# Kernel tuning notes

Measured on AMD Instinct MI355X. Metric: run time of the kernel, lower is better.

## Reference

```python
import jax, jax.numpy as jnp
import numpy as np

N = 32768      # total nodes
E = 262144     # total edges
B = 32         # graphs in batch
NP = N // B    # nodes per graph (equal-sized graphs)
K = 820        # ceil(0.8 * NP), PyG TopKPooling k
H, C = 8, 64   # heads, per-head channels
NEG_SLOPE = 0.2


def setup_inputs() -> dict:
    key = jax.random.key(0)
    ks = jax.random.split(key, 12)
    s = 0.05
    return {
        "x": jax.random.normal(ks[0], (N, 256), jnp.float32),
        "edge_attr": jax.random.normal(ks[1], (E, 32), jnp.float32),
        "Wl": jax.random.normal(ks[2], (256, H * C), jnp.float32) * s,
        "bl": jax.random.normal(ks[3], (H * C,), jnp.float32) * s,
        "Wr": jax.random.normal(ks[4], (256, H * C), jnp.float32) * s,
        "br": jax.random.normal(ks[5], (H * C,), jnp.float32) * s,
        "We": jax.random.normal(ks[6], (32, H * C), jnp.float32) * s,
        "att": jax.random.normal(ks[7], (H, C), jnp.float32) * s,
        "bias": jax.random.normal(ks[8], (H * C,), jnp.float32) * s,
        "pool_w": jax.random.normal(ks[9], (H * C,), jnp.float32),
        "edge_index": jax.random.randint(ks[10], (2, E), 0, N, jnp.int32),
    }


def reference(x, edge_attr, Wl, bl, Wr, br, We, att, bias, pool_w, edge_index):
    src, dst = edge_index[0], edge_index[1]
    # GATv2Conv (eval mode, dropout off)
    xl = (x @ Wl + bl).reshape(N, H, C)   # x_j side (lin_l)
    xr = (x @ Wr + br).reshape(N, H, C)   # x_i side (lin_r)
    e = (edge_attr @ We).reshape(E, H, C)  # lin_edge, bias=False
    m = jax.nn.leaky_relu(xl[src] + xr[dst] + e, NEG_SLOPE)   # [E,H,C]
    alpha = jnp.einsum('ehc,hc->eh', m, att)                  # [E,H]
    amax = jax.ops.segment_max(alpha, dst, num_segments=N)
    ex = jnp.exp(alpha - amax[dst])
    denom = jax.ops.segment_sum(ex, dst, num_segments=N)
    alpha = ex / denom[dst]                                   # segment softmax over dst
    out = jax.ops.segment_sum(alpha[..., None] * xl[src], dst, num_segments=N)
    h = jax.nn.relu(out.reshape(N, H * C) + bias)             # [N,512]
    # TopKPooling: score = tanh(x.w / ||w||), keep top-k per graph, scale kept rows
    score = jnp.tanh(h @ pool_w / jnp.sqrt(jnp.sum(pool_w * pool_w)))
    vals, idx = jax.lax.top_k(score.reshape(B, NP), K)        # [B,K]
    hg = h.reshape(B, NP, H * C)
    hsel = jnp.take_along_axis(hg, idx[..., None], axis=1) * vals[..., None]  # [B,K,512]
    # global max pool || global mean pool
    gmp = hsel.max(axis=1)
    gap = hsel.mean(axis=1)
    return jnp.concatenate([gmp, gap], axis=1)                # [B,1024]
```

## Files before the change

### kernel.cpp

```cpp
#include <hip/hip_runtime.h>
#include <hip/hip_bf16.h>
#include <cstdint>
#include <cstddef>

#define N_NODES 32768
#define N_EDGES 262144
#define BGRAPH  32
#define NPG     1024
#define KSEL    820
#define NEG     0.2f

#define BM 128
#define BN 128
#define BK 16

__global__ __launch_bounds__(256) void gemm_xlxr(
    const float* __restrict__ x,
    const float* __restrict__ Wl, const float* __restrict__ bl,
    const float* __restrict__ Wr, const float* __restrict__ br,
    float* __restrict__ xl, float* __restrict__ xr)
{
    __shared__ float As[BK][BM];
    __shared__ float Bs[BK][BN];

    const int bm = blockIdx.x;
    const int bn = blockIdx.y;
    const float* W; const float* bias; float* out; int colbase;
    if (bn < 4) { W = Wl; bias = bl; out = xl; colbase = bn * 128; }
    else        { W = Wr; bias = br; out = xr; colbase = (bn - 4) * 128; }

    const int tid = threadIdx.x;
    const int tm = tid >> 4;
    const int tn = tid & 15;

    float acc[8][8];
#pragma unroll
    for (int i = 0; i < 8; ++i)
#pragma unroll
        for (int j = 0; j < 8; ++j) acc[i][j] = 0.f;

    for (int k0 = 0; k0 < 256; k0 += BK) {
        __syncthreads();
#pragma unroll
        for (int p = 0; p < 2; ++p) {
            int id  = tid + p * 256;
            int row = id >> 2;
            int kc  = (id & 3) << 2;
            float4 v = *(const float4*)&x[(size_t)(bm * BM + row) * 256 + k0 + kc];
            As[kc + 0][row] = v.x; As[kc + 1][row] = v.y;
            As[kc + 2][row] = v.z; As[kc + 3][row] = v.w;
        }
#pragma unroll
        for (int p = 0; p < 2; ++p) {
            int id = tid + p * 256;
            int kk = id >> 5;
            int nf = (id & 31) << 2;
            float4 v = *(const float4*)&W[(size_t)(k0 + kk) * 512 + colbase + nf];
            *(float4*)&Bs[kk][nf] = v;
        }
        __syncthreads();
#pragma unroll
        for (int kk = 0; kk < BK; ++kk) {
            float a[8], b[8];
            *(float4*)&a[0] = *(const float4*)&As[kk][tm * 8];
            *(float4*)&a[4] = *(const float4*)&As[kk][tm * 8 + 4];
            *(float4*)&b[0] = *(const float4*)&Bs[kk][tn * 8];
            *(float4*)&b[4] = *(const float4*)&Bs[kk][tn * 8 + 4];
#pragma unroll
            for (int i = 0; i < 8; ++i)
#pragma unroll
                for (int j = 0; j < 8; ++j) acc[i][j] += a[i] * b[j];
        }
    }

    float bv[8];
    *(float4*)&bv[0] = *(const float4*)&bias[colbase + tn * 8];
    *(float4*)&bv[4] = *(const float4*)&bias[colbase + tn * 8 + 4];
#pragma unroll
    for (int i = 0; i < 8; ++i) {
        int row = bm * BM + tm * 8 + i;
        float4 o0 = make_float4(acc[i][0] + bv[0], acc[i][1] + bv[1],
                                acc[i][2] + bv[2], acc[i][3] + bv[3]);
        float4 o1 = make_float4(acc[i][4] + bv[4], acc[i][5] + bv[5],
                                acc[i][6] + bv[6], acc[i][7] + bv[7]);
        *(float4*)&out[(size_t)row * 512 + colbase + tn * 8]     = o0;
        *(float4*)&out[(size_t)row * 512 + colbase + tn * 8 + 4] = o1;
    }
}

__global__ void k_hist(const int* __restrict__ ei, int* __restrict__ counts)
{
    int e = blockIdx.x * 256 + threadIdx.x;
    if (e < N_EDGES) atomicAdd(&counts[ei[N_EDGES + e]], 1);
}

__global__ __launch_bounds__(1024) void k_scan(
    const int* __restrict__ counts, int* __restrict__ offsets, int* __restrict__ cursors)
{
    __shared__ int part[1024];
    const int tid = threadIdx.x;
    const int base = tid * 32;
    int loc[32];
    int s = 0;
#pragma unroll
    for (int i = 0; i < 32; ++i) { loc[i] = s; s += counts[base + i]; }
    part[tid] = s;
    __syncthreads();
    const int own = s;
    for (int off = 1; off < 1024; off <<= 1) {
        int v = (tid >= off) ? part[tid - off] : 0;
        __syncthreads();
        part[tid] += v;
        __syncthreads();
    }
    const int pre = part[tid] - own;
#pragma unroll
    for (int i = 0; i < 32; ++i) {
        int o = pre + loc[i];
        offsets[base + i] = o;
        cursors[base + i] = o;
    }
}

__global__ void k_scatter(const int* __restrict__ ei, int* __restrict__ cursors,
                          int* __restrict__ sorted_src, int* __restrict__ sorted_eid)
{
    int e = blockIdx.x * 256 + threadIdx.x;
    if (e >= N_EDGES) return;
    int d = ei[N_EDGES + e];
    int pos = atomicAdd(&cursors[d], 1);
    sorted_src[pos] = ei[e];
    sorted_eid[pos] = e;
}

__global__ void k_gather_ea(const int* __restrict__ sorted_eid,
                            const float* __restrict__ ea, float* __restrict__ sorted_ea)
{
    int pos = blockIdx.x * 8 + (threadIdx.x >> 5);
    int col = threadIdx.x & 31;
    int e = sorted_eid[pos];
    sorted_ea[(size_t)pos * 32 + col] = ea[(size_t)e * 32 + col];
}

#define DPW 8

__global__ __launch_bounds__(128) void k_edge_agg(
    const float* __restrict__ xl, const float* __restrict__ xr,
    const float* __restrict__ We, const float* __restrict__ att,
    const float* __restrict__ bias, const float* __restrict__ pw,
    const float* __restrict__ sorted_ea, const int* __restrict__ sorted_src,
    const int* __restrict__ offsets, const int* __restrict__ counts,
    float* __restrict__ h, float* __restrict__ score)
{
    __shared__ float red_s[2];

    const int tid = threadIdx.x;
    const int wv  = tid >> 6;
    const int l   = tid & 63;
    const int cbase = wv * 256 + l * 4;

    float4 wreg[32];
#pragma unroll
    for (int k = 0; k < 32; ++k)
        wreg[k] = *(const float4*)&We[k * 512 + cbase];

    const float4 attv = *(const float4*)&att[cbase];
    const float4 bv   = *(const float4*)&bias[cbase];
    const float4 pwv  = *(const float4*)&pw[cbase];

    float nrm = pwv.x*pwv.x + pwv.y*pwv.y + pwv.z*pwv.z + pwv.w*pwv.w;
#pragma unroll
    for (int o = 1; o < 64; o <<= 1) nrm += __shfl_xor(nrm, o);
    if (l == 0) red_s[wv] = nrm;
    __syncthreads();
    const float inv_nrm = 1.0f / sqrtf(red_s[0] + red_s[1]);

    for (int dd = 0; dd < DPW; ++dd) {
        const int d   = blockIdx.x * DPW + dd;
        const int off = offsets[d];
        const int deg = counts[d];
        const float4 xr4 = *(const float4*)&xr[(size_t)d * 512 + cbase];

        float m = -INFINITY, den = 0.f;
        float a0 = 0.f, a1 = 0.f, a2 = 0.f, a3 = 0.f;

        for (int j = 0; j < deg; ++j) {
            const int s = sorted_src[off + j];
            const float4 xl4 = *(const float4*)&xl[(size_t)s * 512 + cbase];
            const float* eap = &sorted_ea[(size_t)(off + j) * 32];

            float d0 = 0.f, d1 = 0.f, d2 = 0.f, d3 = 0.f;
#pragma unroll
            for (int k = 0; k < 32; ++k) {
                const float e = eap[k];
                d0 += e * wreg[k].x; d1 += e * wreg[k].y;
                d2 += e * wreg[k].z; d3 += e * wreg[k].w;
            }
            float t0 = xl4.x + xr4.x + d0; t0 = t0 > 0.f ? t0 : NEG * t0;
            float t1 = xl4.y + xr4.y + d1; t1 = t1 > 0.f ? t1 : NEG * t1;
            float t2 = xl4.z + xr4.z + d2; t2 = t2 > 0.f ? t2 : NEG * t2;
            float t3 = xl4.w + xr4.w + d3; t3 = t3 > 0.f ? t3 : NEG * t3;

            float p = t0 * attv.x + t1 * attv.y + t2 * attv.z + t3 * attv.w;
#pragma unroll
            for (int o = 1; o < 16; o <<= 1) p += __shfl_xor(p, o);

            const float mn = fmaxf(m, p);
            const float sc = __expf(m - mn);
            const float pe = __expf(p - mn);
            den = den * sc + pe;
            a0 = a0 * sc + pe * xl4.x;
            a1 = a1 * sc + pe * xl4.y;
            a2 = a2 * sc + pe * xl4.z;
            a3 = a3 * sc + pe * xl4.w;
            m = mn;
        }

        const float r = den > 0.f ? 1.0f / den : 0.f;
        const float h0 = fmaxf(a0 * r + bv.x, 0.f);
        const float h1 = fmaxf(a1 * r + bv.y, 0.f);
        const float h2 = fmaxf(a2 * r + bv.z, 0.f);
        const float h3 = fmaxf(a3 * r + bv.w, 0.f);
        *(float4*)&h[(size_t)d * 512 + cbase] = make_float4(h0, h1, h2, h3);

        float ps = h0 * pwv.x + h1 * pwv.y + h2 * pwv.z + h3 * pwv.w;
#pragma unroll
        for (int o = 1; o < 64; o <<= 1) ps += __shfl_xor(ps, o);
        __syncthreads();
        if (l == 0) red_s[wv] = ps;
        __syncthreads();
        if (tid == 0) score[d] = tanhf((red_s[0] + red_s[1]) * inv_nrm);
    }
}

__global__ __launch_bounds__(256) void k_topk(const float* __restrict__ score,
                                              int* __restrict__ sel_idx,
                                              float* __restrict__ sel_val)
{
    __shared__ unsigned long long key[1024];
    const int g = blockIdx.x, tid = threadIdx.x;
    for (int i = tid; i < 1024; i += 256) {
        float s = score[g * 1024 + i];
        unsigned u = __float_as_uint(s);
        u = (u & 0x80000000u) ? ~u : (u | 0x80000000u);
        key[i] = ((unsigned long long)(~u) << 32) | (unsigned)i;
    }
    __syncthreads();
    for (int k = 2; k <= 1024; k <<= 1) {
        for (int j = k >> 1; j > 0; j >>= 1) {
            for (int i = tid; i < 1024; i += 256) {
                int ixj = i ^ j;
                if (ixj > i) {
                    bool up = ((i & k) == 0);
                    unsigned long long a = key[i], b = key[ixj];
                    if ((a > b) == up) { key[i] = b; key[ixj] = a; }
                }
            }
            __syncthreads();
        }
    }
    for (int kk = tid; kk < KSEL; kk += 256) {
        int idx = (int)(key[kk] & 0xFFFFFFFFu);
        sel_idx[g * KSEL + kk] = idx;
        sel_val[g * KSEL + kk] = score[g * 1024 + idx];
    }
}

#define KSLICE 103

__global__ __launch_bounds__(256) void k_pool_part(
    const float* __restrict__ h, const int* __restrict__ sel_idx,
    const float* __restrict__ sel_val, float* __restrict__ part)
{
    const int g = blockIdx.x >> 3, sl = blockIdx.x & 7;
    const int kbeg = sl * KSLICE;
    const int kend = min(KSEL, kbeg + KSLICE);
    const int n = kend - kbeg;
    __shared__ float vs[KSLICE];
    __shared__ int   is_[KSLICE];
    const int tid = threadIdx.x;
    if (tid < n) {
        vs[tid]  = sel_val[g * KSEL + kbeg + tid];
        is_[tid] = sel_idx[g * KSEL + kbeg + tid];
    }
    __syncthreads();
    const int c0 = tid, c1 = tid + 256;
    float mx0 = -INFINITY, mx1 = -INFINITY, s0 = 0.f, s1 = 0.f;
    for (int kk = 0; kk < n; ++kk) {
        const float* hp = h + ((size_t)(g * 1024 + is_[kk])) * 512;
        const float v = vs[kk];
        float f0 = hp[c0] * v, f1 = hp[c1] * v;
        mx0 = fmaxf(mx0, f0); s0 += f0;
        mx1 = fmaxf(mx1, f1); s1 += f1;
    }
    const size_t base = ((size_t)blockIdx.x * 2) * 512;
    part[base + c0] = mx0;        part[base + c1] = mx1;
    part[base + 512 + c0] = s0;   part[base + 512 + c1] = s1;
}

__global__ __launch_bounds__(256) void k_pool_merge(
    const float* __restrict__ part, float* __restrict__ out)
{
    const int g = blockIdx.x, tid = threadIdx.x;
    const int c0 = tid, c1 = tid + 256;
    float mx0 = -INFINITY, mx1 = -INFINITY, s0 = 0.f, s1 = 0.f;
    for (int sl = 0; sl < 8; ++sl) {
        const size_t base = ((size_t)(g * 8 + sl) * 2) * 512;
        mx0 = fmaxf(mx0, part[base + c0]); mx1 = fmaxf(mx1, part[base + c1]);
        s0 += part[base + 512 + c0];       s1 += part[base + 512 + c1];
    }
    out[(size_t)g * 1024 + c0] = mx0;
    out[(size_t)g * 1024 + c1] = mx1;
    out[(size_t)g * 1024 + 512 + c0] = s0 * (1.f / KSEL);
    out[(size_t)g * 1024 + 512 + c1] = s1 * (1.f / KSEL);
}

extern "C" void kernel_launch(void* const* d_in, const int* in_sizes, int n_in,
                              void* d_out, int out_size, void* d_ws, size_t ws_size,
                              hipStream_t stream)
{
    const float* x    = (const float*)d_in[0];
    const float* ea   = (const float*)d_in[1];
    const float* Wl   = (const float*)d_in[2];
    const float* bl   = (const float*)d_in[3];
    const float* Wr   = (const float*)d_in[4];
    const float* br   = (const float*)d_in[5];
    const float* We   = (const float*)d_in[6];
    const float* att  = (const float*)d_in[7];
    const float* bias = (const float*)d_in[8];
    const float* pw   = (const float*)d_in[9];
    const int*   ei   = (const int*)d_in[10];
    float* out = (float*)d_out;

    float* xl        = (float*)d_ws;
    float* xr        = xl + (size_t)N_NODES * 512;
    float* h         = xr + (size_t)N_NODES * 512;
    float* sorted_ea = h + (size_t)N_NODES * 512;
    float* sel_val   = sorted_ea + (size_t)N_EDGES * 32;
    float* part      = sel_val + BGRAPH * KSEL;
    float* score     = part + 256 * 2 * 512;
    int* counts      = (int*)(score + N_NODES);
    int* offsets     = counts + N_NODES;
    int* cursors     = offsets + N_NODES;
    int* sorted_src  = cursors + N_NODES;
    int* sorted_eid  = sorted_src + N_EDGES;
    int* sel_idx     = sorted_eid + N_EDGES;

    hipMemsetAsync(counts, 0, (size_t)N_NODES * sizeof(int), stream);

    gemm_xlxr<<<dim3(256, 8), 256, 0, stream>>>(x, Wl, bl, Wr, br, xl, xr);
    k_hist<<<N_EDGES / 256, 256, 0, stream>>>(ei, counts);
    k_scan<<<1, 1024, 0, stream>>>(counts, offsets, cursors);
    k_scatter<<<N_EDGES / 256, 256, 0, stream>>>(ei, cursors, sorted_src, sorted_eid);
    k_gather_ea<<<N_EDGES / 8, 256, 0, stream>>>(sorted_eid, ea, sorted_ea);
    k_edge_agg<<<N_NODES / DPW, 128, 0, stream>>>(xl, xr, We, att, bias, pw,
                                                  sorted_ea, sorted_src, offsets, counts,
                                                  h, score);
    k_topk<<<BGRAPH, 256, 0, stream>>>(score, sel_idx, sel_val);
    k_pool_part<<<BGRAPH * 8, 256, 0, stream>>>(h, sel_idx, sel_val, part);
    k_pool_merge<<<BGRAPH, 256, 0, stream>>>(part, out);
}
```

Before: 651.0 us.

## Split edge aggregation into per-edge logit kernel and per-node softmax aggregation

Replaces the fused per-destination online-softmax kernel with two kernels. The first computes the attention logits per edge, parallelized over edges, and reads edge_attr directly through the edge id, so the separate sorted_ea gather kernel is dropped. The second does a two-pass softmax per destination over the stored logits and gathers xl again. This makes the logit work independent of node degree, at the cost of an extra logits buffer, a second xl gather and an extra pass over the logits.

```diff
diff --git a/kernel.cpp b/kernel.cpp
--- a/kernel.cpp
+++ b/kernel.cpp
@@ -123,113 +123,139 @@
 }
 
 __global__ void k_scatter(const int* __restrict__ ei, int* __restrict__ cursors,
-                          int* __restrict__ sorted_src, int* __restrict__ sorted_eid)
+                          int* __restrict__ sorted_src, int* __restrict__ sorted_dst,
+                          int* __restrict__ sorted_eid)
 {
     int e = blockIdx.x * 256 + threadIdx.x;
     if (e >= N_EDGES) return;
     int d = ei[N_EDGES + e];
     int pos = atomicAdd(&cursors[d], 1);
     sorted_src[pos] = ei[e];
+    sorted_dst[pos] = d;
     sorted_eid[pos] = e;
 }
 
-__global__ void k_gather_ea(const int* __restrict__ sorted_eid,
-                            const float* __restrict__ ea, float* __restrict__ sorted_ea)
-{
-    int pos = blockIdx.x * 8 + (threadIdx.x >> 5);
-    int col = threadIdx.x & 31;
-    int e = sorted_eid[pos];
-    sorted_ea[(size_t)pos * 32 + col] = ea[(size_t)e * 32 + col];
-}
-
-#define DPW 8
-
-__global__ __launch_bounds__(128) void k_edge_agg(
+#define EPB 32
+
+__global__ __launch_bounds__(256, 4) void k_alpha(
     const float* __restrict__ xl, const float* __restrict__ xr,
-    const float* __restrict__ We, const float* __restrict__ att,
+    const float* __restrict__ ea, const float* __restrict__ We,
+    const float* __restrict__ att,
+    const int* __restrict__ sorted_src, const int* __restrict__ sorted_dst,
+    const int* __restrict__ sorted_eid,
+    float* __restrict__ logits)
+{
+    const int tid = threadIdx.x;
+    const int c0 = tid * 2;
+    const int head = tid >> 5;
+    const int lead = ((tid & 31) == 0);
+
+    float2 wr[32];
+#pragma unroll
+    for (int k = 0; k < 32; ++k)
+        wr[k] = *(const float2*)&We[k * 512 + c0];
+    const float2 attv = *(const float2*)&att[c0];
+
+    const int p0 = blockIdx.x * EPB;
+    for (int j = 0; j < EPB; j += 2) {
+        const int pA = p0 + j, pB = p0 + j + 1;
+        const int sA = sorted_src[pA], sB = sorted_src[pB];
+        const int dA = sorted_dst[pA], dB = sorted_dst[pB];
+        const int eA = sorted_eid[pA], eB = sorted_eid[pB];
+        const float2 xlA = *(const float2*)&xl[(size_t)sA * 512 + c0];
+        const float2 xrA = *(const float2*)&xr[(size_t)dA * 512 + c0];
+        const float2 xlB = *(const float2*)&xl[(size_t)sB * 512 + c0];
+        const float2 xrB = *(const float2*)&xr[(size_t)dB * 512 + c0];
+        const float* eaA = &ea[(size_t)eA * 32];
+        const float* eaB = &ea[(size_t)eB * 32];
+
+        float a0 = 0.f, a1 = 0.f, b0 = 0.f, b1 = 0.f;
+#pragma unroll
+        for (int k = 0; k < 32; ++k) {
+            const float evA = eaA[k];
+            const float evB = eaB[k];
+            a0 += evA * wr[k].x; a1 += evA * wr[k].y;
+            b0 += evB * wr[k].x; b1 += evB * wr[k].y;
+        }
+        float tA0 = xlA.x + xrA.x + a0; tA0 = tA0 > 0.f ? tA0 : NEG * tA0;
+        float tA1 = xlA.y + xrA.y + a1; tA1 = tA1 > 0.f ? tA1 : NEG * tA1;
+        float tB0 = xlB.x + xrB.x + b0; tB0 = tB0 > 0.f ? tB0 : NEG * tB0;
+        float tB1 = xlB.y + xrB.y + b1; tB1 = tB1 > 0.f ? tB1 : NEG * tB1;
+
+        float lA = tA0 * attv.x + tA1 * attv.y;
+        float lB = tB0 * attv.x + tB1 * attv.y;
+#pragma unroll
+        for (int o = 1; o < 32; o <<= 1) {
+            lA += __shfl_xor(lA, o);
+            lB += __shfl_xor(lB, o);
+        }
+        if (lead) {
+            logits[(size_t)pA * 8 + head] = lA;
+            logits[(size_t)pB * 8 + head] = lB;
+        }
+    }
+}
+
+#define AGG_DPB 8
+
+__global__ __launch_bounds__(256, 8) void k_agg(
+    const float* __restrict__ xl, const float* __restrict__ logits,
+    const int* __restrict__ sorted_src,
+    const int* __restrict__ offsets, const int* __restrict__ counts,
     const float* __restrict__ bias, const float* __restrict__ pw,
-    const float* __restrict__ sorted_ea, const int* __restrict__ sorted_src,
-    const int* __restrict__ offsets, const int* __restrict__ counts,
     float* __restrict__ h, float* __restrict__ score)
 {
-    __shared__ float red_s[2];
+    __shared__ float red_s[4];
 
     const int tid = threadIdx.x;
     const int wv  = tid >> 6;
     const int l   = tid & 63;
-    const int cbase = wv * 256 + l * 4;
-
-    float4 wreg[32];
-#pragma unroll
-    for (int k = 0; k < 32; ++k)
-        wreg[k] = *(const float4*)&We[k * 512 + cbase];
-
-    const float4 attv = *(const float4*)&att[cbase];
-    const float4 bv   = *(const float4*)&bias[cbase];
-    const float4 pwv  = *(const float4*)&pw[cbase];
-
-    float nrm = pwv.x*pwv.x + pwv.y*pwv.y + pwv.z*pwv.z + pwv.w*pwv.w;
+    const int c0  = tid * 2;
+    const int head = tid >> 5;
+
+    const float2 bv  = *(const float2*)&bias[c0];
+    const float2 pwv = *(const float2*)&pw[c0];
+
+    float nrm = pwv.x * pwv.x + pwv.y * pwv.y;
 #pragma unroll
     for (int o = 1; o < 64; o <<= 1) nrm += __shfl_xor(nrm, o);
     if (l == 0) red_s[wv] = nrm;
     __syncthreads();
-    const float inv_nrm = 1.0f / sqrtf(red_s[0] + red_s[1]);
-
-    for (int dd = 0; dd < DPW; ++dd) {
-        const int d   = blockIdx.x * DPW + dd;
+    const float inv_nrm = 1.0f / sqrtf(red_s[0] + red_s[1] + red_s[2] + red_s[3]);
+
+    for (int dd = 0; dd < AGG_DPB; ++dd) {
+        const int d   = blockIdx.x * AGG_DPB + dd;
         const int off = offsets[d];
         const int deg = counts[d];
-        const float4 xr4 = *(const float4*)&xr[(size_t)d * 512 + cbase];
-
-        float m = -INFINITY, den = 0.f;
-        float a0 = 0.f, a1 = 0.f, a2 = 0.f, a3 = 0.f;
-
+
+        float m = -INFINITY;
+        for (int j = 0; j < deg; ++j)
+            m = fmaxf(m, logits[(size_t)(off + j) * 8 + head]);
+
+        float den = 0.f, a0 = 0.f, a1 = 0.f;
         for (int j = 0; j < deg; ++j) {
-            const int s = sorted_src[off + j];
-            const float4 xl4 = *(const float4*)&xl[(size_t)s * 512 + cbase];
-            const float* eap = &sorted_ea[(size_t)(off + j) * 32];
-
-            float d0 = 0.f, d1 = 0.f, d2 = 0.f, d3 = 0.f;
-#pragma unroll
-            for (int k = 0; k < 32; ++k) {
-                const float e = eap[k];
-                d0 += e * wreg[k].x; d1 += e * wreg[k].y;
-                d2 += e * wreg[k].z; d3 += e * wreg[k].w;
-            }
-            float t0 = xl4.x + xr4.x + d0; t0 = t0 > 0.f ? t0 : NEG * t0;
-            float t1 = xl4.y + xr4.y + d1; t1 = t1 > 0.f ? t1 : NEG * t1;
-            float t2 = xl4.z + xr4.z + d2; t2 = t2 > 0.f ? t2 : NEG * t2;
-            float t3 = xl4.w + xr4.w + d3; t3 = t3 > 0.f ? t3 : NEG * t3;
-
-            float p = t0 * attv.x + t1 * attv.y + t2 * attv.z + t3 * attv.w;
-#pragma unroll
-            for (int o = 1; o < 16; o <<= 1) p += __shfl_xor(p, o);
-
-            const float mn = fmaxf(m, p);
-            const float sc = __expf(m - mn);
-            const float pe = __expf(p - mn);
-            den = den * sc + pe;
-            a0 = a0 * sc + pe * xl4.x;
-            a1 = a1 * sc + pe * xl4.y;
-            a2 = a2 * sc + pe * xl4.z;
-            a3 = a3 * sc + pe * xl4.w;
-            m = mn;
+            const float lg = logits[(size_t)(off + j) * 8 + head];
+            const int   s  = sorted_src[off + j];
+            const float2 xl2 = *(const float2*)&xl[(size_t)s * 512 + c0];
+            const float pe = __expf(lg - m);
+            den += pe;
+            a0 += pe * xl2.x;
+            a1 += pe * xl2.y;
         }
 
         const float r = den > 0.f ? 1.0f / den : 0.f;
         const float h0 = fmaxf(a0 * r + bv.x, 0.f);
         const float h1 = fmaxf(a1 * r + bv.y, 0.f);
-        const float h2 = fmaxf(a2 * r + bv.z, 0.f);
-        const float h3 = fmaxf(a3 * r + bv.w, 0.f);
-        *(float4*)&h[(size_t)d * 512 + cbase] = make_float4(h0, h1, h2, h3);
-
-        float ps = h0 * pwv.x + h1 * pwv.y + h2 * pwv.z + h3 * pwv.w;
+        *(float2*)&h[(size_t)d * 512 + c0] = make_float2(h0, h1);
+
+        float ps = h0 * pwv.x + h1 * pwv.y;
 #pragma unroll
         for (int o = 1; o < 64; o <<= 1) ps += __shfl_xor(ps, o);
         __syncthreads();
         if (l == 0) red_s[wv] = ps;
         __syncthreads();
-        if (tid == 0) score[d] = tanhf((red_s[0] + red_s[1]) * inv_nrm);
+        if (tid == 0)
+            score[d] = tanhf((red_s[0] + red_s[1] + red_s[2] + red_s[3]) * inv_nrm);
     }
 }
 
@@ -335,15 +361,16 @@
     float* xl        = (float*)d_ws;
     float* xr        = xl + (size_t)N_NODES * 512;
     float* h         = xr + (size_t)N_NODES * 512;
-    float* sorted_ea = h + (size_t)N_NODES * 512;
-    float* sel_val   = sorted_ea + (size_t)N_EDGES * 32;
+    float* logits    = h + (size_t)N_NODES * 512;
+    float* sel_val   = logits + (size_t)N_EDGES * 8;
     float* part      = sel_val + BGRAPH * KSEL;
     float* score     = part + 256 * 2 * 512;
     int* counts      = (int*)(score + N_NODES);
     int* offsets     = counts + N_NODES;
     int* cursors     = offsets + N_NODES;
     int* sorted_src  = cursors + N_NODES;
-    int* sorted_eid  = sorted_src + N_EDGES;
+    int* sorted_dst  = sorted_src + N_EDGES;
+    int* sorted_eid  = sorted_dst + N_EDGES;
     int* sel_idx     = sorted_eid + N_EDGES;
 
     hipMemsetAsync(counts, 0, (size_t)N_NODES * sizeof(int), stream);
@@ -351,11 +378,11 @@
     gemm_xlxr<<<dim3(256, 8), 256, 0, stream>>>(x, Wl, bl, Wr, br, xl, xr);
     k_hist<<<N_EDGES / 256, 256, 0, stream>>>(ei, counts);
     k_scan<<<1, 1024, 0, stream>>>(counts, offsets, cursors);
-    k_scatter<<<N_EDGES / 256, 256, 0, stream>>>(ei, cursors, sorted_src, sorted_eid);
-    k_gather_ea<<<N_EDGES / 8, 256, 0, stream>>>(sorted_eid, ea, sorted_ea);
-    k_edge_agg<<<N_NODES / DPW, 128, 0, stream>>>(xl, xr, We, att, bias, pw,
-                                                  sorted_ea, sorted_src, offsets, counts,
-                                                  h, score);
+    k_scatter<<<N_EDGES / 256, 256, 0, stream>>>(ei, cursors, sorted_src, sorted_dst, sorted_eid);
+    k_alpha<<<N_EDGES / EPB, 256, 0, stream>>>(xl, xr, ea, We, att,
+                                               sorted_src, sorted_dst, sorted_eid, logits);
+    k_agg<<<N_NODES / AGG_DPB, 256, 0, stream>>>(xl, logits, sorted_src, offsets, counts,
+                                                 bias, pw, h, score);
     k_topk<<<BGRAPH, 256, 0, stream>>>(score, sel_idx, sel_val);
     k_pool_part<<<BGRAPH * 8, 256, 0, stream>>>(h, sel_idx, sel_val, part);
     k_pool_merge<<<BGRAPH, 256, 0, stream>>>(part, out);
```

Measured after the change: 744.1 us. 1.14x slower.
